# Performance work log

Measured on AMD Instinct MI355X. Metric: run time of the kernel, lower is better.

The kernel has to match this reference:

```python
import jax, jax.numpy as jnp
import numpy as np

B, H, T, N = 8, 12, 1024, 256  # N = mlp_internal_dim_multiplier * n_embd // n_head = 4*768//12
THETA = 2.0 ** 16


def _rope(phases, v):
    # interleaved rotate-half: pairs (even, odd) -> (-odd, even), as in torch stack+view
    v_rot = jnp.stack((-v[..., 1::2], v[..., ::2]), axis=-1).reshape(v.shape)
    ang = (phases % 1.0) * (2.0 * jnp.pi)
    return v * jnp.cos(ang) + v_rot * jnp.sin(ang)


def setup_inputs() -> dict:
    key = jax.random.key(0)
    k1, k2 = jax.random.split(key)
    Q = jax.random.normal(k1, (B, H, T, N), dtype=jnp.float32)
    V = jax.random.normal(k2, (B, H, T, N), dtype=jnp.float32)
    # frozen RoPE frequency buffer: pairs share a frequency, theta=2**16 (cycles/position)
    idx = (jnp.arange(N) // 2 * 2).astype(jnp.float32)
    freqs = (THETA ** (-idx / N)).reshape(1, 1, 1, N)
    return {"Q": Q, "V": V, "freqs": freqs}


def reference(Q, V, freqs):
    t = Q.shape[2]
    pos = jnp.arange(t, dtype=freqs.dtype).reshape(1, 1, -1, 1)
    phases = pos * freqs                      # [1,1,T,N]
    QR = _rope(phases, Q)                     # K is Q in Vision-BDH, so KR = QR
    scale = 1.0 / jnp.sqrt(jnp.asarray(Q.shape[-1], Q.dtype))
    scores = jnp.einsum("bhtn,bhsn->bhts", QR, QR) * scale  # [B,H,T,T]
    attn = jax.nn.softmax(scores, axis=-1)
    return jnp.einsum("bhts,bhsn->bhtn", attn, V)
```

## Files before the change

kernel.cpp:

```cpp
#include <hip/hip_runtime.h>
#include <stdint.h>

typedef __attribute__((ext_vector_type(8))) short short8;
typedef __attribute__((ext_vector_type(4))) float f32x4;

#define BH 96
#define T 1024
#define D 256

static __device__ __forceinline__ unsigned short f2bf(float x){
  uint32_t u = __float_as_uint(x);
  uint32_t r = (u + 0x7FFFu + ((u >> 16) & 1u)) >> 16;
  return (unsigned short)r;
}

static __device__ __forceinline__ uint32_t cvtpk_bf16(float lo, float hi){
  uint32_t r;
  asm("v_cvt_pk_bf16_f32 %0, %1, %2" : "=v"(r) : "v"(lo), "v"(hi));
  return r;
}

static __device__ __forceinline__ float exp2_fast(float x){
  float r;
  asm("v_exp_f32 %0, %1" : "=v"(r) : "v"(x));
  return r;
}

static __device__ __forceinline__ void gload_lds16(const void* g, void* l){
  __builtin_amdgcn_global_load_lds((const __attribute__((address_space(1))) void*)g,
                                   (__attribute__((address_space(3))) void*)l, 16, 0, 0);
}

__global__ void k_rope(const float* __restrict__ Q, const float* __restrict__ freqs,
                       unsigned short* __restrict__ QR){
  const float SC = 0.25f * 1.20112241f;
  long idx = (long)blockIdx.x * 256 + threadIdx.x;
  long e = idx * 4;
  int n = (int)(e & (D - 1));
  int t = (int)((e >> 8) & (T - 1));
  float4 q = *(const float4*)(Q + e);
  float f0 = freqs[n];
  float f2 = freqs[n + 2];
  float ph0 = (float)t * f0; ph0 -= floorf(ph0);
  float ph2 = (float)t * f2; ph2 -= floorf(ph2);
  float c0 = __builtin_amdgcn_cosf(ph0), s0 = __builtin_amdgcn_sinf(ph0);
  float c2 = __builtin_amdgcn_cosf(ph2), s2 = __builtin_amdgcn_sinf(ph2);
  float o0 = (q.x * c0 - q.y * s0) * SC;
  float o1 = (q.y * c0 + q.x * s0) * SC;
  float o2 = (q.z * c2 - q.w * s2) * SC;
  float o3 = (q.w * c2 + q.z * s2) * SC;
  ushort4 o;
  o.x = f2bf(o0); o.y = f2bf(o1); o.z = f2bf(o2); o.w = f2bf(o3);
  *(ushort4*)(QR + e) = o;
}

__global__ void k_transpose(const float* __restrict__ V, unsigned short* __restrict__ Vt){
  __shared__ unsigned short L[64 * 66];
  int bid = blockIdx.x;
  int head = bid >> 6;
  int rem = bid & 63;
  int t0 = (rem & 15) * 64;
  int n0 = (rem >> 4) * 64;
  int tid = threadIdx.x;
  const float* Vh = V + (long)head * T * D;
  unsigned short* Vth = Vt + (long)head * T * D;
  int lr = tid >> 4;
  int lc = (tid & 15) * 4;
#pragma unroll
  for (int i = 0; i < 4; ++i){
    int tl = i * 16 + lr;
    float4 v = *(const float4*)(Vh + (long)(t0 + tl) * D + n0 + lc);
    uint32_t w0 = (uint32_t)f2bf(v.x) | ((uint32_t)f2bf(v.y) << 16);
    uint32_t w1 = (uint32_t)f2bf(v.z) | ((uint32_t)f2bf(v.w) << 16);
    *(uint32_t*)&L[tl * 66 + lc]     = w0;
    *(uint32_t*)&L[tl * 66 + lc + 2] = w1;
  }
  __syncthreads();
  int nr = tid >> 3;
  int t8 = (tid & 7) * 8;
#pragma unroll
  for (int i = 0; i < 2; ++i){
    int n_row = i * 32 + nr;
    unsigned short u[8];
#pragma unroll
    for (int j = 0; j < 8; ++j) u[j] = L[(t8 + j) * 66 + n_row];
    uint4 o;
    o.x = (uint32_t)u[0] | ((uint32_t)u[1] << 16);
    o.y = (uint32_t)u[2] | ((uint32_t)u[3] << 16);
    o.z = (uint32_t)u[4] | ((uint32_t)u[5] << 16);
    o.w = (uint32_t)u[6] | ((uint32_t)u[7] << 16);
    *(uint4*)(Vth + (long)(n0 + n_row) * T + t0 + t8) = o;
  }
}

static __device__ __forceinline__ short8 softmax_step(
    f32x4 st0, f32x4 st1, float& m, float& lsum, f32x4* acc, int q15, int g)
{
  float lm = fmaxf(fmaxf(fmaxf(st0.x, st0.y), fmaxf(st0.z, st0.w)),
                   fmaxf(fmaxf(st1.x, st1.y), fmaxf(st1.z, st1.w)));
  if (__any(lm > m + 11.0f)){
    float tm = fmaxf(lm, __shfl_xor(lm, 16));
    tm = fmaxf(tm, __shfl_xor(tm, 32));
    float mnew = fmaxf(m, tm);
    float alpha = exp2_fast(m - mnew);
    float a0 = __shfl(alpha, g * 4 + 0);
    float a1 = __shfl(alpha, g * 4 + 1);
    float a2 = __shfl(alpha, g * 4 + 2);
    float a3 = __shfl(alpha, g * 4 + 3);
#pragma unroll
    for (int nc = 0; nc < 16; ++nc){
      acc[nc].x *= a0; acc[nc].y *= a1; acc[nc].z *= a2; acc[nc].w *= a3;
    }
    lsum *= alpha;
    m = mnew;
  }
  float p00 = exp2_fast(st0.x - m), p01 = exp2_fast(st0.y - m);
  float p02 = exp2_fast(st0.z - m), p03 = exp2_fast(st0.w - m);
  float p10 = exp2_fast(st1.x - m), p11 = exp2_fast(st1.y - m);
  float p12 = exp2_fast(st1.z - m), p13 = exp2_fast(st1.w - m);
  float ts = ((p00 + p01) + (p02 + p03)) + ((p10 + p11) + (p12 + p13));
  ts += __shfl_xor(ts, 16);
  ts += __shfl_xor(ts, 32);
  lsum += ts;
  uint32_t t0w0 = cvtpk_bf16(p00, p01), t0w1 = cvtpk_bf16(p02, p03);
  uint32_t t1w0 = cvtpk_bf16(p10, p11), t1w1 = cvtpk_bf16(p12, p13);
  int s0l = ((g & 1) << 5) | q15;
  int s1l = s0l + 16;
  uint32_t x0 = __shfl(t0w0, s0l), x1 = __shfl(t0w1, s0l);
  uint32_t X0 = __shfl(t1w0, s0l), X1 = __shfl(t1w1, s0l);
  uint32_t y0 = __shfl(t0w0, s1l), y1 = __shfl(t0w1, s1l);
  uint32_t Y0 = __shfl(t1w0, s1l), Y1 = __shfl(t1w1, s1l);
  bool lo = (g < 2);
  uint4 aws;
  aws.x = lo ? x0 : X0;
  aws.y = lo ? x1 : X1;
  aws.z = lo ? y0 : Y0;
  aws.w = lo ? y1 : Y1;
  return __builtin_bit_cast(short8, aws);
}

__global__ __launch_bounds__(256, 2) void k_flash(const unsigned short* __restrict__ QR,
                                                  const unsigned short* __restrict__ Vt,
                                                  float* __restrict__ Out){
  __shared__ short lds[2][16384];
  int tid = threadIdx.x;
  int wid = tid >> 6, lane = tid & 63;
  int q15 = lane & 15, g = lane >> 4;

  int b = blockIdx.x;
  int x = b & 7, s = b >> 3;
  int qt = s & 7, hg = s >> 3;
  int head = hg * 8 + x;

  const unsigned short* qr = QR + (long)head * T * D;
  const unsigned short* vt = Vt + (long)head * T * D;
  int qb = qt * 128 + wid * 32;

  int bK[4], bV[4];
#pragma unroll
  for (int j = 0; j < 4; ++j){
    int i = tid + j * 256;
    bK[j] = (((i >> 9) * 16 + (i & 15)) * 256) + ((i >> 6) & 7) * 32 + ((i >> 4) & 3) * 8;
    bV[j] = ((i >> 6) * 16 + (i & 15)) * 1024 + ((i >> 4) & 3) * 8;
  }

  short8 qfA[8], qfB[8];
#pragma unroll
  for (int c = 0; c < 8; ++c){
    qfA[c] = *(const short8*)(qr + (long)(qb + q15) * D + c * 32 + g * 8);
    qfB[c] = *(const short8*)(qr + (long)(qb + 16 + q15) * D + c * 32 + g * 8);
  }

  f32x4 accA[16], accB[16];
#pragma unroll
  for (int i = 0; i < 16; ++i){
    accA[i] = f32x4{0.f, 0.f, 0.f, 0.f};
    accB[i] = f32x4{0.f, 0.f, 0.f, 0.f};
  }
  float mA = -3e38f, mB = -3e38f, lA = 0.f, lB = 0.f;

#pragma unroll
  for (int j = 0; j < 4; ++j){
    int i = tid + j * 256;
    gload_lds16(qr + bK[j], &lds[0][i * 8]);
    gload_lds16(vt + bV[j], &lds[0][8192 + i * 8]);
  }
  asm volatile("s_waitcnt vmcnt(0)" ::: "memory");
  __syncthreads();

  int buf = 0;
  for (int kb = 0; kb < T; kb += 32){
    if (kb + 32 < T){
      const unsigned short* sk = qr + (long)(kb + 32) * 256;
      const unsigned short* sv = vt + (kb + 32);
#pragma unroll
      for (int j = 0; j < 4; ++j){
        int i = tid + j * 256;
        gload_lds16(sk + bK[j], &lds[buf ^ 1][i * 8]);
        gload_lds16(sv + bV[j], &lds[buf ^ 1][8192 + i * 8]);
      }
    }
    const short* ldsK = &lds[buf][0];
    const short* ldsV = &lds[buf][8192];

    f32x4 s0a = f32x4{0.f,0.f,0.f,0.f}, s0b = f32x4{0.f,0.f,0.f,0.f};
    f32x4 s1a = f32x4{0.f,0.f,0.f,0.f}, s1b = f32x4{0.f,0.f,0.f,0.f};
#pragma unroll
    for (int c = 0; c < 8; ++c){
      short8 kf0 = *(const short8*)&ldsK[c * 512 + lane * 8];
      short8 kf1 = *(const short8*)&ldsK[4096 + c * 512 + lane * 8];
      s0a = __builtin_amdgcn_mfma_f32_16x16x32_bf16(kf0, qfA[c], s0a, 0, 0, 0);
      s0b = __builtin_amdgcn_mfma_f32_16x16x32_bf16(kf0, qfB[c], s0b, 0, 0, 0);
      s1a = __builtin_amdgcn_mfma_f32_16x16x32_bf16(kf1, qfA[c], s1a, 0, 0, 0);
      s1b = __builtin_amdgcn_mfma_f32_16x16x32_bf16(kf1, qfB[c], s1b, 0, 0, 0);
    }
    short8 paA = softmax_step(s0a, s1a, mA, lA, accA, q15, g);
    short8 paB = softmax_step(s0b, s1b, mB, lB, accB, q15, g);
#pragma unroll
    for (int nc = 0; nc < 16; ++nc){
      short8 vf = *(const short8*)&ldsV[nc * 512 + lane * 8];
      accA[nc] = __builtin_amdgcn_mfma_f32_16x16x32_bf16(paA, vf, accA[nc], 0, 0, 0);
      accB[nc] = __builtin_amdgcn_mfma_f32_16x16x32_bf16(paB, vf, accB[nc], 0, 0, 0);
    }
    asm volatile("s_waitcnt vmcnt(0)" ::: "memory");
    __syncthreads();
    buf ^= 1;
  }

  float* op = Out + (long)head * T * D + (long)qb * D;
  {
    float rl = 1.0f / lA;
    float d0 = __shfl(rl, g * 4 + 0);
    float d1 = __shfl(rl, g * 4 + 1);
    float d2 = __shfl(rl, g * 4 + 2);
    float d3 = __shfl(rl, g * 4 + 3);
#pragma unroll
    for (int nc = 0; nc < 16; ++nc){
      float* o = op + nc * 16 + q15;
      o[(g * 4 + 0) * D] = accA[nc].x * d0;
      o[(g * 4 + 1) * D] = accA[nc].y * d1;
      o[(g * 4 + 2) * D] = accA[nc].z * d2;
      o[(g * 4 + 3) * D] = accA[nc].w * d3;
    }
  }
  {
    float rl = 1.0f / lB;
    float d0 = __shfl(rl, g * 4 + 0);
    float d1 = __shfl(rl, g * 4 + 1);
    float d2 = __shfl(rl, g * 4 + 2);
    float d3 = __shfl(rl, g * 4 + 3);
    float* o2 = op + 16 * D;
#pragma unroll
    for (int nc = 0; nc < 16; ++nc){
      float* o = o2 + nc * 16 + q15;
      o[(g * 4 + 0) * D] = accB[nc].x * d0;
      o[(g * 4 + 1) * D] = accB[nc].y * d1;
      o[(g * 4 + 2) * D] = accB[nc].z * d2;
      o[(g * 4 + 3) * D] = accB[nc].w * d3;
    }
  }
}

extern "C" void kernel_launch(void* const* d_in, const int* in_sizes, int n_in,
                              void* d_out, int out_size, void* d_ws, size_t ws_size,
                              hipStream_t stream){
  (void)in_sizes; (void)n_in; (void)out_size; (void)ws_size;
  const float* Q     = (const float*)d_in[0];
  const float* V     = (const float*)d_in[1];
  const float* freqs = (const float*)d_in[2];
  float* Out = (float*)d_out;
  unsigned short* QR = (unsigned short*)d_ws;
  unsigned short* Vt = QR + (size_t)BH * T * D;
  k_rope<<<dim3((BH * T * D) / 4 / 256), dim3(256), 0, stream>>>(Q, freqs, QR);
  k_transpose<<<dim3(BH * 64), dim3(256), 0, stream>>>(V, Vt);
  k_flash<<<dim3(BH * 8), dim3(256), 0, stream>>>(QR, Vt, Out);
}
```

Before: 189.8 us.

## Software-pipeline flash loop: overlap QK of next tile with PV of previous

Restructures the attention main loop so each iteration computes QK^T for the current key tile and then P·V for the previous tile, with separate double buffers for K and V in LDS. Operands of the PV MFMA are swapped so the accumulator layout is transposed, which removes the alpha shuffles and enables vectorized f32x4 output stores. The row sum reduction across lanes is deferred to the end, and s_setprio is raised around MFMA blocks. This aims to hide softmax latency behind matrix work, at the cost of more complex buffer indexing and keeping the P fragments live across iterations.

```diff
diff --git a/kernel.cpp b/kernel.cpp
--- a/kernel.cpp
+++ b/kernel.cpp
@@ -93,35 +93,13 @@
   }
 }
 
-static __device__ __forceinline__ short8 softmax_step(
-    f32x4 st0, f32x4 st1, float& m, float& lsum, f32x4* acc, int q15, int g)
-{
-  float lm = fmaxf(fmaxf(fmaxf(st0.x, st0.y), fmaxf(st0.z, st0.w)),
-                   fmaxf(fmaxf(st1.x, st1.y), fmaxf(st1.z, st1.w)));
-  if (__any(lm > m + 11.0f)){
-    float tm = fmaxf(lm, __shfl_xor(lm, 16));
-    tm = fmaxf(tm, __shfl_xor(tm, 32));
-    float mnew = fmaxf(m, tm);
-    float alpha = exp2_fast(m - mnew);
-    float a0 = __shfl(alpha, g * 4 + 0);
-    float a1 = __shfl(alpha, g * 4 + 1);
-    float a2 = __shfl(alpha, g * 4 + 2);
-    float a3 = __shfl(alpha, g * 4 + 3);
-#pragma unroll
-    for (int nc = 0; nc < 16; ++nc){
-      acc[nc].x *= a0; acc[nc].y *= a1; acc[nc].z *= a2; acc[nc].w *= a3;
-    }
-    lsum *= alpha;
-    m = mnew;
-  }
+static __device__ __forceinline__ short8 packP(f32x4 st0, f32x4 st1, float m, float& lsum,
+                                               int q15, int g){
   float p00 = exp2_fast(st0.x - m), p01 = exp2_fast(st0.y - m);
   float p02 = exp2_fast(st0.z - m), p03 = exp2_fast(st0.w - m);
   float p10 = exp2_fast(st1.x - m), p11 = exp2_fast(st1.y - m);
   float p12 = exp2_fast(st1.z - m), p13 = exp2_fast(st1.w - m);
-  float ts = ((p00 + p01) + (p02 + p03)) + ((p10 + p11) + (p12 + p13));
-  ts += __shfl_xor(ts, 16);
-  ts += __shfl_xor(ts, 32);
-  lsum += ts;
+  lsum += ((p00 + p01) + (p02 + p03)) + ((p10 + p11) + (p12 + p13));
   uint32_t t0w0 = cvtpk_bf16(p00, p01), t0w1 = cvtpk_bf16(p02, p03);
   uint32_t t1w0 = cvtpk_bf16(p10, p11), t1w1 = cvtpk_bf16(p12, p13);
   int s0l = ((g & 1) << 5) | q15;
@@ -139,10 +117,32 @@
   return __builtin_bit_cast(short8, aws);
 }
 
+static __device__ __forceinline__ void softmax2(
+    f32x4 s0a, f32x4 s1a, f32x4 s0b, f32x4 s1b,
+    float& mA, float& mB, float& lA, float& lB,
+    f32x4* accA, f32x4* accB, short8& paA, short8& paB, int q15, int g){
+  float lmA = fmaxf(fmaxf(fmaxf(s0a.x, s0a.y), fmaxf(s0a.z, s0a.w)),
+                    fmaxf(fmaxf(s1a.x, s1a.y), fmaxf(s1a.z, s1a.w)));
+  float lmB = fmaxf(fmaxf(fmaxf(s0b.x, s0b.y), fmaxf(s0b.z, s0b.w)),
+                    fmaxf(fmaxf(s1b.x, s1b.y), fmaxf(s1b.z, s1b.w)));
+  if (__any((lmA > mA + 11.0f) || (lmB > mB + 11.0f))){
+    float tmA = fmaxf(lmA, __shfl_xor(lmA, 16)); tmA = fmaxf(tmA, __shfl_xor(tmA, 32));
+    float tmB = fmaxf(lmB, __shfl_xor(lmB, 16)); tmB = fmaxf(tmB, __shfl_xor(tmB, 32));
+    float mnA = fmaxf(mA, tmA), mnB = fmaxf(mB, tmB);
+    float aA = exp2_fast(mA - mnA), aB = exp2_fast(mB - mnB);
+    mA = mnA; mB = mnB;
+    lA *= aA; lB *= aB;
+#pragma unroll
+    for (int nc = 0; nc < 16; ++nc){ accA[nc] *= aA; accB[nc] *= aB; }
+  }
+  paA = packP(s0a, s1a, mA, lA, q15, g);
+  paB = packP(s0b, s1b, mB, lB, q15, g);
+}
+
 __global__ __launch_bounds__(256, 2) void k_flash(const unsigned short* __restrict__ QR,
                                                   const unsigned short* __restrict__ Vt,
                                                   float* __restrict__ Out){
-  __shared__ short lds[2][16384];
+  __shared__ short lds[4][8192];
   int tid = threadIdx.x;
   int wid = tid >> 6, lane = tid & 63;
   int q15 = lane & 15, g = lane >> 4;
@@ -178,33 +178,27 @@
     accB[i] = f32x4{0.f, 0.f, 0.f, 0.f};
   }
   float mA = -3e38f, mB = -3e38f, lA = 0.f, lB = 0.f;
+  short8 paA, paB;
 
 #pragma unroll
   for (int j = 0; j < 4; ++j){
     int i = tid + j * 256;
     gload_lds16(qr + bK[j], &lds[0][i * 8]);
-    gload_lds16(vt + bV[j], &lds[0][8192 + i * 8]);
   }
   asm volatile("s_waitcnt vmcnt(0)" ::: "memory");
   __syncthreads();
 
-  int buf = 0;
-  for (int kb = 0; kb < T; kb += 32){
-    if (kb + 32 < T){
-      const unsigned short* sk = qr + (long)(kb + 32) * 256;
-      const unsigned short* sv = vt + (kb + 32);
-#pragma unroll
-      for (int j = 0; j < 4; ++j){
-        int i = tid + j * 256;
-        gload_lds16(sk + bK[j], &lds[buf ^ 1][i * 8]);
-        gload_lds16(sv + bV[j], &lds[buf ^ 1][8192 + i * 8]);
-      }
-    }
-    const short* ldsK = &lds[buf][0];
-    const short* ldsV = &lds[buf][8192];
-
+  {
+#pragma unroll
+    for (int j = 0; j < 4; ++j){
+      int i = tid + j * 256;
+      gload_lds16(qr + 32 * 256 + bK[j], &lds[1][i * 8]);
+      gload_lds16(vt + bV[j],            &lds[2][i * 8]);
+    }
+    const short* ldsK = lds[0];
     f32x4 s0a = f32x4{0.f,0.f,0.f,0.f}, s0b = f32x4{0.f,0.f,0.f,0.f};
     f32x4 s1a = f32x4{0.f,0.f,0.f,0.f}, s1b = f32x4{0.f,0.f,0.f,0.f};
+    __builtin_amdgcn_s_setprio(1);
 #pragma unroll
     for (int c = 0; c < 8; ++c){
       short8 kf0 = *(const short8*)&ldsK[c * 512 + lane * 8];
@@ -214,50 +208,75 @@
       s1a = __builtin_amdgcn_mfma_f32_16x16x32_bf16(kf1, qfA[c], s1a, 0, 0, 0);
       s1b = __builtin_amdgcn_mfma_f32_16x16x32_bf16(kf1, qfB[c], s1b, 0, 0, 0);
     }
-    short8 paA = softmax_step(s0a, s1a, mA, lA, accA, q15, g);
-    short8 paB = softmax_step(s0b, s1b, mB, lB, accB, q15, g);
-#pragma unroll
-    for (int nc = 0; nc < 16; ++nc){
-      short8 vf = *(const short8*)&ldsV[nc * 512 + lane * 8];
-      accA[nc] = __builtin_amdgcn_mfma_f32_16x16x32_bf16(paA, vf, accA[nc], 0, 0, 0);
-      accB[nc] = __builtin_amdgcn_mfma_f32_16x16x32_bf16(paB, vf, accB[nc], 0, 0, 0);
-    }
+    __builtin_amdgcn_s_setprio(0);
+    softmax2(s0a, s1a, s0b, s1b, mA, mB, lA, lB, accA, accB, paA, paB, q15, g);
     asm volatile("s_waitcnt vmcnt(0)" ::: "memory");
     __syncthreads();
-    buf ^= 1;
-  }
-
-  float* op = Out + (long)head * T * D + (long)qb * D;
+  }
+
+  for (int t = 1; t < 32; ++t){
+    int kb = t << 5;
+    {
+      const unsigned short* sk = qr + (long)(kb + 32) * 256;
+      const unsigned short* sv = vt + kb;
+      short* kd = lds[(t + 1) & 1];
+      short* vd = lds[2 + (t & 1)];
+#pragma unroll
+      for (int j = 0; j < 4; ++j){
+        int i = tid + j * 256;
+        gload_lds16(sk + bK[j], kd + i * 8);
+        gload_lds16(sv + bV[j], vd + i * 8);
+      }
+    }
+    const short* ldsK = lds[t & 1];
+    f32x4 s0a = f32x4{0.f,0.f,0.f,0.f}, s0b = f32x4{0.f,0.f,0.f,0.f};
+    f32x4 s1a = f32x4{0.f,0.f,0.f,0.f}, s1b = f32x4{0.f,0.f,0.f,0.f};
+    __builtin_amdgcn_s_setprio(1);
+#pragma unroll
+    for (int c = 0; c < 8; ++c){
+      short8 kf0 = *(const short8*)&ldsK[c * 512 + lane * 8];
+      short8 kf1 = *(const short8*)&ldsK[4096 + c * 512 + lane * 8];
+      s0a = __builtin_amdgcn_mfma_f32_16x16x32_bf16(kf0, qfA[c], s0a, 0, 0, 0);
+      s0b = __builtin_amdgcn_mfma_f32_16x16x32_bf16(kf0, qfB[c], s0b, 0, 0, 0);
+      s1a = __builtin_amdgcn_mfma_f32_16x16x32_bf16(kf1, qfA[c], s1a, 0, 0, 0);
+      s1b = __builtin_amdgcn_mfma_f32_16x16x32_bf16(kf1, qfB[c], s1b, 0, 0, 0);
+    }
+    const short* ldsVp = lds[2 + ((t - 1) & 1)];
+#pragma unroll
+    for (int nc = 0; nc < 16; ++nc){
+      short8 vf = *(const short8*)&ldsVp[nc * 512 + lane * 8];
+      accA[nc] = __builtin_amdgcn_mfma_f32_16x16x32_bf16(vf, paA, accA[nc], 0, 0, 0);
+      accB[nc] = __builtin_amdgcn_mfma_f32_16x16x32_bf16(vf, paB, accB[nc], 0, 0, 0);
+    }
+    __builtin_amdgcn_s_setprio(0);
+    softmax2(s0a, s1a, s0b, s1b, mA, mB, lA, lB, accA, accB, paA, paB, q15, g);
+    asm volatile("s_waitcnt vmcnt(0)" ::: "memory");
+    __syncthreads();
+  }
+
   {
-    float rl = 1.0f / lA;
-    float d0 = __shfl(rl, g * 4 + 0);
-    float d1 = __shfl(rl, g * 4 + 1);
-    float d2 = __shfl(rl, g * 4 + 2);
-    float d3 = __shfl(rl, g * 4 + 3);
+    const short* ldsVp = lds[3];
+    __builtin_amdgcn_s_setprio(1);
 #pragma unroll
     for (int nc = 0; nc < 16; ++nc){
-      float* o = op + nc * 16 + q15;
-      o[(g * 4 + 0) * D] = accA[nc].x * d0;
-      o[(g * 4 + 1) * D] = accA[nc].y * d1;
-      o[(g * 4 + 2) * D] = accA[nc].z * d2;
-      o[(g * 4 + 3) * D] = accA[nc].w * d3;
-    }
-  }
-  {
-    float rl = 1.0f / lB;
-    float d0 = __shfl(rl, g * 4 + 0);
-    float d1 = __shfl(rl, g * 4 + 1);
-    float d2 = __shfl(rl, g * 4 + 2);
-    float d3 = __shfl(rl, g * 4 + 3);
-    float* o2 = op + 16 * D;
-#pragma unroll
-    for (int nc = 0; nc < 16; ++nc){
-      float* o = o2 + nc * 16 + q15;
-      o[(g * 4 + 0) * D] = accB[nc].x * d0;
-      o[(g * 4 + 1) * D] = accB[nc].y * d1;
-      o[(g * 4 + 2) * D] = accB[nc].z * d2;
-      o[(g * 4 + 3) * D] = accB[nc].w * d3;
-    }
+      short8 vf = *(const short8*)&ldsVp[nc * 512 + lane * 8];
+      accA[nc] = __builtin_amdgcn_mfma_f32_16x16x32_bf16(vf, paA, accA[nc], 0, 0, 0);
+      accB[nc] = __builtin_amdgcn_mfma_f32_16x16x32_bf16(vf, paB, accB[nc], 0, 0, 0);
+    }
+    __builtin_amdgcn_s_setprio(0);
+  }
+
+  lA += __shfl_xor(lA, 16); lA += __shfl_xor(lA, 32);
+  lB += __shfl_xor(lB, 16); lB += __shfl_xor(lB, 32);
+  float rA = 1.0f / lA, rB = 1.0f / lB;
+  float* opA = Out + (long)head * T * D + (long)(qb + q15) * D + g * 4;
+  float* opB = opA + 16 * D;
+#pragma unroll
+  for (int nc = 0; nc < 16; ++nc){
+    f32x4 oa = accA[nc] * rA;
+    f32x4 ob = accB[nc] * rB;
+    *(f32x4*)(opA + nc * 16) = oa;
+    *(f32x4*)(opB + nc * 16) = ob;
   }
 }
 
```

Result: slower. 268.9 us (+41.7%).
